# Performance work log

Hardware: AMD Instinct MI355X
Metric: run time of the kernel (lower is better)

The kernel has to match this reference:

```python
import jax, jax.numpy as jnp
import numpy as np

B, H, S, D = 2, 12, 2048, 64

def setup_inputs() -> dict:
    key = jax.random.key(0)
    kq, kk, kv = jax.random.split(key, 3)
    Q = jax.random.normal(kq, (B, H, S, D), dtype=jnp.float32)
    K = jax.random.normal(kk, (B, H, S, D), dtype=jnp.float32)
    V = jax.random.normal(kv, (B, H, S, D), dtype=jnp.float32)
    return {"Q": Q, "K": K, "V": V}

def reference(Q, K, V):
    # NOTE: original code scales by sqrt(Q.shape[-2]) (the sequence length),
    # not the head dim — reproduced faithfully.
    scale = 1.0 / np.sqrt(Q.shape[-2]).astype(np.float32)
    scores = jnp.einsum('bhqd,bhkd->bhqk', Q, K) * scale  # [B,H,S,S]
    attn = jax.nn.softmax(scores, axis=-1)
    context = jnp.einsum('bhqk,bhkd->bhqd', attn, V)      # [B,H,S,D]
    # torch .squeeze(-1) only removes the last dim if it is size 1; D=64 so no-op
    return context
```

## Files before the change

### kernel.cpp

```cpp
#include <hip/hip_runtime.h>
#include <hip/hip_bf16.h>
#include <math.h>
#include <stdint.h>

#define BATCH 2
#define NH 12
#define SEQ 2048
#define HD 64
#define TQ 64
#define TK 64
#define NHEADS (BATCH*NH)
#define NIT (SEQ / TK)

typedef short bf16x8 __attribute__((ext_vector_type(8)));
typedef float f32x4 __attribute__((ext_vector_type(4)));
typedef unsigned short us8_t __attribute__((ext_vector_type(8)));

#if __has_builtin(__builtin_amdgcn_exp2f)
#define EXP2F(x) __builtin_amdgcn_exp2f(x)
#else
#define EXP2F(x) exp2f(x)
#endif

static __device__ __forceinline__ unsigned short f2bf(float f) {
    unsigned int u = __float_as_uint(f);
    u += 0x7fffu + ((u >> 16) & 1u);
    return (unsigned short)(u >> 16);
}

static __device__ __forceinline__ unsigned int pack2bf(float a, float b) {
    __hip_bfloat162 v = __float22bfloat162_rn(float2{a, b});
    return *(unsigned int*)&v;
}

static __device__ __forceinline__ void async_cp16(const void* g, void* l) {
    __builtin_amdgcn_global_load_lds(
        (const __attribute__((address_space(1))) void*)g,
        (__attribute__((address_space(3))) void*)(uintptr_t)l,
        16, 0, 0);
}

__global__ __launch_bounds__(256)
void prep_qkv(const float* __restrict__ Q, const float* __restrict__ K,
              const float* __restrict__ V,
              unsigned short* __restrict__ Qb, unsigned short* __restrict__ Kb,
              unsigned short* __restrict__ Vtb, float qs) {
    const int bh = blockIdx.x >> 5;
    const int s0 = (blockIdx.x & 31) * 64;
    const int tid = threadIdx.x;
    const size_t off = ((size_t)bh * SEQ + s0) * HD;

    #pragma unroll
    for (int i = 0; i < 2; ++i) {
        size_t e0 = off + (size_t)(tid + 256 * i) * 8;
        float4 a = *(const float4*)&Q[e0];
        float4 b = *(const float4*)&Q[e0 + 4];
        us8_t rq = { f2bf(a.x*qs), f2bf(a.y*qs), f2bf(a.z*qs), f2bf(a.w*qs),
                     f2bf(b.x*qs), f2bf(b.y*qs), f2bf(b.z*qs), f2bf(b.w*qs) };
        *(us8_t*)&Qb[e0] = rq;
        float4 c = *(const float4*)&K[e0];
        float4 d = *(const float4*)&K[e0 + 4];
        us8_t rk = { f2bf(c.x), f2bf(c.y), f2bf(c.z), f2bf(c.w),
                     f2bf(d.x), f2bf(d.y), f2bf(d.z), f2bf(d.w) };
        *(us8_t*)&Kb[e0] = rk;
    }

    const float* Vsrc = V + off;
    unsigned short* Vdst = Vtb + (size_t)bh * HD * SEQ;
    const int n  = tid & 63;
    const int cg = tid >> 6;
    #pragma unroll
    for (int i = 0; i < 4; ++i) {
        int c4 = (cg + 4 * i) * 4;
        float4 v = *(const float4*)&Vsrc[(size_t)n * HD + c4];
        Vdst[(size_t)(c4 + 0) * SEQ + s0 + n] = f2bf(v.x);
        Vdst[(size_t)(c4 + 1) * SEQ + s0 + n] = f2bf(v.y);
        Vdst[(size_t)(c4 + 2) * SEQ + s0 + n] = f2bf(v.z);
        Vdst[(size_t)(c4 + 3) * SEQ + s0 + n] = f2bf(v.w);
    }
}

__global__ __launch_bounds__(128)
void fa_main(const unsigned short* __restrict__ Qb,
             const unsigned short* __restrict__ Kb,
             const unsigned short* __restrict__ Vtb,
             float* __restrict__ O) {
    const int x  = blockIdx.x & 7;
    const int t  = blockIdx.x >> 3;
    const int bh = x + 8 * (t % 3);
    const int qt = t / 3;
    const int q0 = qt * TQ;

    __shared__ unsigned short Ks[TK * HD];
    __shared__ unsigned short Vs[HD * TK];
    __shared__ unsigned short QP[2 * 32 * 72];
    __shared__ float Lw[2][32];

    const int tid  = threadIdx.x;
    const int w    = tid >> 6;
    const int lane = tid & 63;
    const int col  = lane & 15;
    const int quad = lane >> 4;
    const int r8   = lane >> 3;
    const int c8   = lane & 7;
    const int swz  = col & 7;

    const unsigned short* Qh = Qb  + ((size_t)bh * SEQ + q0) * HD;
    const unsigned short* Kh = Kb  + (size_t)bh * SEQ * HD;
    const unsigned short* Vh = Vtb + (size_t)bh * HD * SEQ;

    #pragma unroll
    for (int i = 0; i < 4; ++i) {
        const int R = w * 32 + i * 8;
        async_cp16(Qh + (size_t)(R + r8) * HD + (c8 ^ r8) * 8, &QP[R * HD]);
    }
    #pragma unroll
    for (int i = 0; i < 4; ++i) {
        const int R = w * 32 + i * 8;
        async_cp16(Kh + (size_t)(R + r8) * HD + (c8 ^ r8) * 8, &Ks[R * HD]);
        async_cp16(Vh + (size_t)(R + r8) * SEQ + (c8 ^ r8) * 8, &Vs[R * HD]);
    }
    __syncthreads();

    bf16x8 qf[2][2];
    #pragma unroll
    for (int mt = 0; mt < 2; ++mt)
        #pragma unroll
        for (int ks = 0; ks < 2; ++ks)
            qf[mt][ks] = *(const bf16x8*)&QP[(w*32 + mt*16 + col) * HD + (((ks*4 + quad) ^ swz) * 8)];
    __syncthreads();

    unsigned short* Psw = &QP[w * 2304];

    f32x4 o[2][4];
    #pragma unroll
    for (int mt = 0; mt < 2; ++mt)
        #pragma unroll
        for (int dt = 0; dt < 4; ++dt) o[mt][dt] = (f32x4){0.f, 0.f, 0.f, 0.f};
    float lsum[2] = {0.f, 0.f};

    for (int it = 0; it < NIT; ++it) {
        f32x4 sc[2][4];
        #pragma unroll
        for (int nt = 0; nt < 4; ++nt) {
            const int kr = (nt*16 + col) * HD;
            bf16x8 kf0 = *(const bf16x8*)&Ks[kr + (((0*4 + quad) ^ swz) * 8)];
            bf16x8 kf1 = *(const bf16x8*)&Ks[kr + (((1*4 + quad) ^ swz) * 8)];
            #pragma unroll
            for (int mt = 0; mt < 2; ++mt) {
                f32x4 z = {0.f, 0.f, 0.f, 0.f};
                z = __builtin_amdgcn_mfma_f32_16x16x32_bf16(kf0, qf[mt][0], z, 0, 0, 0);
                z = __builtin_amdgcn_mfma_f32_16x16x32_bf16(kf1, qf[mt][1], z, 0, 0, 0);
                sc[mt][nt] = z;
            }
        }

        #pragma unroll
        for (int mt = 0; mt < 2; ++mt) {
            #pragma unroll
            for (int nt = 0; nt < 4; ++nt) {
                float p0 = EXP2F(sc[mt][nt][0]);
                float p1 = EXP2F(sc[mt][nt][1]);
                float p2 = EXP2F(sc[mt][nt][2]);
                float p3 = EXP2F(sc[mt][nt][3]);
                lsum[mt] += (p0 + p1) + (p2 + p3);
                uint2 pk = { pack2bf(p0, p1), pack2bf(p2, p3) };
                *(uint2*)&Psw[(mt*16 + col) * 72 + nt*16 + quad*4] = pk;
            }
        }

        bf16x8 pf[2][2];
        #pragma unroll
        for (int mt = 0; mt < 2; ++mt)
            #pragma unroll
            for (int ks = 0; ks < 2; ++ks)
                pf[mt][ks] = *(const bf16x8*)&Psw[(mt*16 + col) * 72 + ks*32 + quad*8];
        #pragma unroll
        for (int dt = 0; dt < 4; ++dt) {
            const int vr = (dt*16 + col) * HD;
            bf16x8 vf0 = *(const bf16x8*)&Vs[vr + (((0*4 + quad) ^ swz) * 8)];
            bf16x8 vf1 = *(const bf16x8*)&Vs[vr + (((1*4 + quad) ^ swz) * 8)];
            #pragma unroll
            for (int mt = 0; mt < 2; ++mt) {
                o[mt][dt] = __builtin_amdgcn_mfma_f32_16x16x32_bf16(pf[mt][0], vf0, o[mt][dt], 0, 0, 0);
                o[mt][dt] = __builtin_amdgcn_mfma_f32_16x16x32_bf16(pf[mt][1], vf1, o[mt][dt], 0, 0, 0);
            }
        }

        __syncthreads();
        if (it + 1 < NIT) {
            const int kv0 = (it + 1) * TK;
            #pragma unroll
            for (int i = 0; i < 4; ++i) {
                const int R = w * 32 + i * 8;
                async_cp16(Kh + (size_t)(kv0 + R + r8) * HD  + (c8 ^ r8) * 8, &Ks[R * HD]);
                async_cp16(Vh + (size_t)(R + r8) * SEQ + kv0 + (c8 ^ r8) * 8, &Vs[R * HD]);
            }
        }
        __syncthreads();
    }

    #pragma unroll
    for (int mt = 0; mt < 2; ++mt) {
        lsum[mt] += __shfl_xor(lsum[mt], 16, 64);
        lsum[mt] += __shfl_xor(lsum[mt], 32, 64);
    }
    if (quad == 0) {
        Lw[w][col]      = lsum[0];
        Lw[w][16 + col] = lsum[1];
    }
    float* Oh = O + ((size_t)bh * SEQ + q0 + w*32) * HD;
    #pragma unroll
    for (int mt = 0; mt < 2; ++mt) {
        #pragma unroll
        for (int r = 0; r < 4; ++r) {
            const int row = mt*16 + quad*4 + r;
            float inv = 1.0f / Lw[w][row];
            #pragma unroll
            for (int dt = 0; dt < 4; ++dt)
                Oh[(size_t)row * HD + dt*16 + col] = o[mt][dt][r] * inv;
        }
    }
}

#define PAD 8
#define LSTR (HD + PAD)

__global__ __launch_bounds__(256)
void fa_fwd_fb(const float* __restrict__ Q, const float* __restrict__ K,
               const float* __restrict__ V, float* __restrict__ O) {
    const int x  = blockIdx.x & 7;
    const int t  = blockIdx.x >> 3;
    const int bh = x + 8 * (t % 3);
    const int qt = t / 3;
    const int q0 = qt * TQ;
    const long base = (long)bh * SEQ * HD;

    __shared__ unsigned short Qs[TQ][LSTR];
    __shared__ unsigned short Ks2[TK][LSTR];
    __shared__ unsigned short Vt[HD][TK + PAD];
    __shared__ unsigned short Ps2[4][16][LSTR];

    const int tid  = threadIdx.x;
    const int wave = tid >> 6;
    const int lane = tid & 63;
    const int col  = lane & 15;
    const int quad = lane >> 4;
    const int m0   = wave * 16;

    #pragma unroll
    for (int i = 0; i < 4; ++i) {
        int idx = tid + 256 * i;
        int row = idx >> 4;
        int c4  = (idx & 15) * 4;
        float4 v = *(const float4*)&Q[base + (long)(q0 + row) * HD + c4];
        ushort4 b = { f2bf(v.x), f2bf(v.y), f2bf(v.z), f2bf(v.w) };
        *(ushort4*)&Qs[row][c4] = b;
    }
    __syncthreads();

    bf16x8 aq0 = *(const bf16x8*)&Qs[m0 + col][quad * 8];
    bf16x8 aq1 = *(const bf16x8*)&Qs[m0 + col][32 + quad * 8];

    f32x4 o0 = {0.f,0.f,0.f,0.f}, o1 = o0, o2 = o0, o3 = o0;
    float l[4] = {0.f, 0.f, 0.f, 0.f};
    const float scale = 0.022097086912079608f;

    for (int kv0 = 0; kv0 < SEQ; kv0 += TK) {
        __syncthreads();
        #pragma unroll
        for (int i = 0; i < 4; ++i) {
            int idx = tid + 256 * i;
            int row = idx >> 4;
            int c4  = (idx & 15) * 4;
            float4 kv = *(const float4*)&K[base + (long)(kv0 + row) * HD + c4];
            ushort4 kb = { f2bf(kv.x), f2bf(kv.y), f2bf(kv.z), f2bf(kv.w) };
            *(ushort4*)&Ks2[row][c4] = kb;
            float4 vv = *(const float4*)&V[base + (long)(kv0 + row) * HD + c4];
            Vt[c4 + 0][row] = f2bf(vv.x);
            Vt[c4 + 1][row] = f2bf(vv.y);
            Vt[c4 + 2][row] = f2bf(vv.z);
            Vt[c4 + 3][row] = f2bf(vv.w);
        }
        __syncthreads();

        f32x4 sc[4];
        #pragma unroll
        for (int n = 0; n < 4; ++n) {
            bf16x8 b0 = *(const bf16x8*)&Ks2[n * 16 + col][quad * 8];
            bf16x8 b1 = *(const bf16x8*)&Ks2[n * 16 + col][32 + quad * 8];
            f32x4 acc = {0.f,0.f,0.f,0.f};
            acc = __builtin_amdgcn_mfma_f32_16x16x32_bf16(aq0, b0, acc, 0, 0, 0);
            acc = __builtin_amdgcn_mfma_f32_16x16x32_bf16(aq1, b1, acc, 0, 0, 0);
            sc[n] = acc;
        }

        float tsum[4] = {0.f, 0.f, 0.f, 0.f};
        #pragma unroll
        for (int n = 0; n < 4; ++n) {
            #pragma unroll
            for (int r = 0; r < 4; ++r) {
                float p = __expf(sc[n][r] * scale);
                tsum[r] += p;
                Ps2[wave][quad * 4 + r][n * 16 + col] = f2bf(p);
            }
        }
        #pragma unroll
        for (int off = 1; off < 16; off <<= 1) {
            #pragma unroll
            for (int r = 0; r < 4; ++r) tsum[r] += __shfl_xor(tsum[r], off, 64);
        }
        #pragma unroll
        for (int r = 0; r < 4; ++r) l[r] += tsum[r];

        bf16x8 ap0 = *(const bf16x8*)&Ps2[wave][col][quad * 8];
        bf16x8 ap1 = *(const bf16x8*)&Ps2[wave][col][32 + quad * 8];
        #pragma unroll
        for (int n = 0; n < 4; ++n) {
            bf16x8 b0 = *(const bf16x8*)&Vt[n * 16 + col][quad * 8];
            bf16x8 b1 = *(const bf16x8*)&Vt[n * 16 + col][32 + quad * 8];
            f32x4* op = (n == 0) ? &o0 : (n == 1) ? &o1 : (n == 2) ? &o2 : &o3;
            *op = __builtin_amdgcn_mfma_f32_16x16x32_bf16(ap0, b0, *op, 0, 0, 0);
            *op = __builtin_amdgcn_mfma_f32_16x16x32_bf16(ap1, b1, *op, 0, 0, 0);
        }
    }

    float inv[4];
    #pragma unroll
    for (int r = 0; r < 4; ++r) inv[r] = 1.0f / l[r];
    #pragma unroll
    for (int r = 0; r < 4; ++r) {
        long row = base + (long)(q0 + m0 + quad * 4 + r) * HD;
        O[row +  0 + col] = o0[r] * inv[r];
        O[row + 16 + col] = o1[r] * inv[r];
        O[row + 32 + col] = o2[r] * inv[r];
        O[row + 48 + col] = o3[r] * inv[r];
    }
}

extern "C" void kernel_launch(void* const* d_in, const int* in_sizes, int n_in,
                              void* d_out, int out_size, void* d_ws, size_t ws_size,
                              hipStream_t stream) {
    const float* Q = (const float*)d_in[0];
    const float* K = (const float*)d_in[1];
    const float* V = (const float*)d_in[2];
    float* O = (float*)d_out;

    const size_t tensorElems = (size_t)NHEADS * SEQ * HD;
    const size_t need = 3 * tensorElems * sizeof(unsigned short);

    if (ws_size >= need) {
        unsigned short* Qb  = (unsigned short*)d_ws;
        unsigned short* Kb  = Qb + tensorElems;
        unsigned short* Vtb = Kb + tensorElems;
        const float qs = (float)(1.4426950408889634 / sqrt(2048.0));
        prep_qkv<<<dim3(NHEADS * (SEQ / 64)), dim3(256), 0, stream>>>(Q, K, V, Qb, Kb, Vtb, qs);
        fa_main<<<dim3(NHEADS * (SEQ / TQ)), dim3(128), 0, stream>>>(Qb, Kb, Vtb, O);
    } else {
        fa_fwd_fb<<<dim3(NHEADS * (SEQ / TQ)), dim3(256), 0, stream>>>(Q, K, V, O);
    }
}
```

Baseline: 140.1 us.

## Split KV tile across four waves with 32x32 MFMA and double-buffered K/V

```diff
diff --git a/kernel.cpp b/kernel.cpp
--- a/kernel.cpp
+++ b/kernel.cpp
@@ -14,6 +14,7 @@
 
 typedef short bf16x8 __attribute__((ext_vector_type(8)));
 typedef float f32x4 __attribute__((ext_vector_type(4)));
+typedef float f32x16 __attribute__((ext_vector_type(16)));
 typedef unsigned short us8_t __attribute__((ext_vector_type(8)));
 
 #if __has_builtin(__builtin_amdgcn_exp2f)
@@ -80,7 +81,7 @@
     }
 }
 
-__global__ __launch_bounds__(128)
+__global__ __launch_bounds__(256)
 void fa_main(const unsigned short* __restrict__ Qb,
              const unsigned short* __restrict__ Kb,
              const unsigned short* __restrict__ Vtb,
@@ -91,134 +92,142 @@
     const int qt = t / 3;
     const int q0 = qt * TQ;
 
-    __shared__ unsigned short Ks[TK * HD];
-    __shared__ unsigned short Vs[HD * TK];
-    __shared__ unsigned short QP[2 * 32 * 72];
-    __shared__ float Lw[2][32];
+    __shared__ unsigned short Ksh[2][TK * HD];
+    __shared__ unsigned short Vsh[2][HD * TK];
+    __shared__ unsigned short Ps[TQ * TK];
+    __shared__ float Lsum[TQ];
+    __shared__ float Linv[TQ];
 
     const int tid  = threadIdx.x;
     const int w    = tid >> 6;
+    const int mt   = w >> 1;
+    const int nt   = w & 1;
     const int lane = tid & 63;
-    const int col  = lane & 15;
-    const int quad = lane >> 4;
+    const int l31  = lane & 31;
+    const int hi   = lane >> 5;
+    const int l7   = lane & 7;
     const int r8   = lane >> 3;
     const int c8   = lane & 7;
-    const int swz  = col & 7;
 
     const unsigned short* Qh = Qb  + ((size_t)bh * SEQ + q0) * HD;
     const unsigned short* Kh = Kb  + (size_t)bh * SEQ * HD;
     const unsigned short* Vh = Vtb + (size_t)bh * HD * SEQ;
 
-    #pragma unroll
-    for (int i = 0; i < 4; ++i) {
-        const int R = w * 32 + i * 8;
-        async_cp16(Qh + (size_t)(R + r8) * HD + (c8 ^ r8) * 8, &QP[R * HD]);
-    }
-    #pragma unroll
-    for (int i = 0; i < 4; ++i) {
-        const int R = w * 32 + i * 8;
-        async_cp16(Kh + (size_t)(R + r8) * HD + (c8 ^ r8) * 8, &Ks[R * HD]);
-        async_cp16(Vh + (size_t)(R + r8) * SEQ + (c8 ^ r8) * 8, &Vs[R * HD]);
+    {
+        const int R = w * 16;
+        async_cp16(Qh + (size_t)(R     + r8) * HD + (c8 ^ r8) * 8, &Ksh[1][ R      * HD]);
+        async_cp16(Qh + (size_t)(R + 8 + r8) * HD + (c8 ^ r8) * 8, &Ksh[1][(R + 8) * HD]);
+        async_cp16(Kh + (size_t)(R     + r8) * HD + (c8 ^ r8) * 8, &Ksh[0][ R      * HD]);
+        async_cp16(Kh + (size_t)(R + 8 + r8) * HD + (c8 ^ r8) * 8, &Ksh[0][(R + 8) * HD]);
+        async_cp16(Vh + (size_t)(R     + r8) * SEQ + (c8 ^ r8) * 8, &Vsh[0][ R      * HD]);
+        async_cp16(Vh + (size_t)(R + 8 + r8) * SEQ + (c8 ^ r8) * 8, &Vsh[0][(R + 8) * HD]);
     }
     __syncthreads();
 
-    bf16x8 qf[2][2];
-    #pragma unroll
-    for (int mt = 0; mt < 2; ++mt)
-        #pragma unroll
-        for (int ks = 0; ks < 2; ++ks)
-            qf[mt][ks] = *(const bf16x8*)&QP[(w*32 + mt*16 + col) * HD + (((ks*4 + quad) ^ swz) * 8)];
+    bf16x8 qf[4];
+    #pragma unroll
+    for (int s = 0; s < 4; ++s)
+        qf[s] = *(const bf16x8*)&Ksh[1][(mt*32 + l31) * HD + (((s*2 + hi) ^ l7) * 8)];
     __syncthreads();
 
-    unsigned short* Psw = &QP[w * 2304];
-
-    f32x4 o[2][4];
-    #pragma unroll
-    for (int mt = 0; mt < 2; ++mt)
-        #pragma unroll
-        for (int dt = 0; dt < 4; ++dt) o[mt][dt] = (f32x4){0.f, 0.f, 0.f, 0.f};
-    float lsum[2] = {0.f, 0.f};
+    f32x16 o[2];
+    o[0] = (f32x16)(0.f);
+    o[1] = (f32x16)(0.f);
+    float lsum = 0.f;
 
     for (int it = 0; it < NIT; ++it) {
-        f32x4 sc[2][4];
-        #pragma unroll
-        for (int nt = 0; nt < 4; ++nt) {
-            const int kr = (nt*16 + col) * HD;
-            bf16x8 kf0 = *(const bf16x8*)&Ks[kr + (((0*4 + quad) ^ swz) * 8)];
-            bf16x8 kf1 = *(const bf16x8*)&Ks[kr + (((1*4 + quad) ^ swz) * 8)];
-            #pragma unroll
-            for (int mt = 0; mt < 2; ++mt) {
-                f32x4 z = {0.f, 0.f, 0.f, 0.f};
-                z = __builtin_amdgcn_mfma_f32_16x16x32_bf16(kf0, qf[mt][0], z, 0, 0, 0);
-                z = __builtin_amdgcn_mfma_f32_16x16x32_bf16(kf1, qf[mt][1], z, 0, 0, 0);
-                sc[mt][nt] = z;
+        const int cur = it & 1;
+        if (it + 1 < NIT) {
+            const int nb  = cur ^ 1;
+            const int kv0 = (it + 1) * TK;
+            const int R   = w * 16;
+            async_cp16(Kh + (size_t)(kv0 + R     + r8) * HD  + (c8 ^ r8) * 8, &Ksh[nb][ R      * HD]);
+            async_cp16(Kh + (size_t)(kv0 + R + 8 + r8) * HD  + (c8 ^ r8) * 8, &Ksh[nb][(R + 8) * HD]);
+            async_cp16(Vh + (size_t)(R     + r8) * SEQ + kv0 + (c8 ^ r8) * 8, &Vsh[nb][ R      * HD]);
+            async_cp16(Vh + (size_t)(R + 8 + r8) * SEQ + kv0 + (c8 ^ r8) * 8, &Vsh[nb][(R + 8) * HD]);
+        }
+        const unsigned short* Ks = Ksh[cur];
+        const unsigned short* Vs = Vsh[cur];
+
+        f32x16 sc = (f32x16)(0.f);
+        #pragma unroll
+        for (int s = 0; s < 4; ++s) {
+            bf16x8 kf = *(const bf16x8*)&Ks[(nt*32 + l31) * HD + (((s*2 + hi) ^ l7) * 8)];
+            sc = __builtin_amdgcn_mfma_f32_32x32x16_bf16(kf, qf[s], sc, 0, 0, 0);
+        }
+
+        float e[16];
+        #pragma unroll
+        for (int r = 0; r < 16; ++r) e[r] = EXP2F(sc[r]);
+        #pragma unroll
+        for (int r = 0; r < 16; ++r) lsum += e[r];
+        #pragma unroll
+        for (int g = 0; g < 4; ++g) {
+            const int m = mt*32 + l31;
+            const int ch = nt*4 + g;
+            uint2 pk = { pack2bf(e[4*g+0], e[4*g+1]), pack2bf(e[4*g+2], e[4*g+3]) };
+            *(uint2*)&Ps[m * TK + ((ch ^ (m & 7)) * 8) + hi * 4] = pk;
+        }
+
+        bf16x8 pf[2];
+        #pragma unroll
+        for (int ks = 0; ks < 2; ++ks) {
+            const int m = mt*32 + l31;
+            const int ch = nt*4 + ks*2 + hi;
+            pf[ks] = *(const bf16x8*)&Ps[m * TK + ((ch ^ (m & 7)) * 8)];
+        }
+        #pragma unroll
+        for (int dt = 0; dt < 2; ++dt) {
+            const int d = dt*32 + l31;
+            #pragma unroll
+            for (int ks = 0; ks < 2; ++ks) {
+                const int ch = nt*4 + ks*2 + hi;
+                bf16x8 vf = *(const bf16x8*)&Vs[d * HD + ((ch ^ l7) * 8)];
+                o[dt] = __builtin_amdgcn_mfma_f32_32x32x16_bf16(pf[ks], vf, o[dt], 0, 0, 0);
             }
         }
 
-        #pragma unroll
-        for (int mt = 0; mt < 2; ++mt) {
-            #pragma unroll
-            for (int nt = 0; nt < 4; ++nt) {
-                float p0 = EXP2F(sc[mt][nt][0]);
-                float p1 = EXP2F(sc[mt][nt][1]);
-                float p2 = EXP2F(sc[mt][nt][2]);
-                float p3 = EXP2F(sc[mt][nt][3]);
-                lsum[mt] += (p0 + p1) + (p2 + p3);
-                uint2 pk = { pack2bf(p0, p1), pack2bf(p2, p3) };
-                *(uint2*)&Psw[(mt*16 + col) * 72 + nt*16 + quad*4] = pk;
+        __syncthreads();
+    }
+
+    lsum += __shfl_xor(lsum, 32, 64);
+    float* ORed = (float*)Ksh;
+
+    if (nt == 1) {
+        if (lane < 32) Lsum[mt*32 + lane] = lsum;
+        #pragma unroll
+        for (int dt = 0; dt < 2; ++dt) {
+            const int d = dt*32 + l31;
+            #pragma unroll
+            for (int g = 0; g < 4; ++g) {
+                const int m0 = mt*32 + 8*g + 4*hi;
+                const int ph = (m0 >> 2) ^ (d & 15);
+                float4 v = { o[dt][4*g+0], o[dt][4*g+1], o[dt][4*g+2], o[dt][4*g+3] };
+                *(float4*)&ORed[d * 64 + ph * 4] = v;
             }
         }
-
-        bf16x8 pf[2][2];
-        #pragma unroll
-        for (int mt = 0; mt < 2; ++mt)
-            #pragma unroll
-            for (int ks = 0; ks < 2; ++ks)
-                pf[mt][ks] = *(const bf16x8*)&Psw[(mt*16 + col) * 72 + ks*32 + quad*8];
-        #pragma unroll
-        for (int dt = 0; dt < 4; ++dt) {
-            const int vr = (dt*16 + col) * HD;
-            bf16x8 vf0 = *(const bf16x8*)&Vs[vr + (((0*4 + quad) ^ swz) * 8)];
-            bf16x8 vf1 = *(const bf16x8*)&Vs[vr + (((1*4 + quad) ^ swz) * 8)];
-            #pragma unroll
-            for (int mt = 0; mt < 2; ++mt) {
-                o[mt][dt] = __builtin_amdgcn_mfma_f32_16x16x32_bf16(pf[mt][0], vf0, o[mt][dt], 0, 0, 0);
-                o[mt][dt] = __builtin_amdgcn_mfma_f32_16x16x32_bf16(pf[mt][1], vf1, o[mt][dt], 0, 0, 0);
+    }
+    __syncthreads();
+
+    if (nt == 0) {
+        float ltot = lsum + Lsum[mt*32 + l31];
+        if (lane < 32) Linv[mt*32 + lane] = 1.0f / ltot;
+        float* Oh = O + ((size_t)bh * SEQ + q0) * HD;
+        #pragma unroll
+        for (int dt = 0; dt < 2; ++dt) {
+            const int d = dt*32 + l31;
+            #pragma unroll
+            for (int g = 0; g < 4; ++g) {
+                const int m0 = mt*32 + 8*g + 4*hi;
+                const int ph = (m0 >> 2) ^ (d & 15);
+                float4 part = *(const float4*)&ORed[d * 64 + ph * 4];
+                float4 inv4 = *(const float4*)&Linv[m0];
+                const float* pp = (const float*)&part;
+                const float* ii = (const float*)&inv4;
+                #pragma unroll
+                for (int j = 0; j < 4; ++j)
+                    Oh[(size_t)(m0 + j) * HD + d] = (o[dt][4*g+j] + pp[j]) * ii[j];
             }
-        }
-
-        __syncthreads();
-        if (it + 1 < NIT) {
-            const int kv0 = (it + 1) * TK;
-            #pragma unroll
-            for (int i = 0; i < 4; ++i) {
-                const int R = w * 32 + i * 8;
-                async_cp16(Kh + (size_t)(kv0 + R + r8) * HD  + (c8 ^ r8) * 8, &Ks[R * HD]);
-                async_cp16(Vh + (size_t)(R + r8) * SEQ + kv0 + (c8 ^ r8) * 8, &Vs[R * HD]);
-            }
-        }
-        __syncthreads();
-    }
-
-    #pragma unroll
-    for (int mt = 0; mt < 2; ++mt) {
-        lsum[mt] += __shfl_xor(lsum[mt], 16, 64);
-        lsum[mt] += __shfl_xor(lsum[mt], 32, 64);
-    }
-    if (quad == 0) {
-        Lw[w][col]      = lsum[0];
-        Lw[w][16 + col] = lsum[1];
-    }
-    float* Oh = O + ((size_t)bh * SEQ + q0 + w*32) * HD;
-    #pragma unroll
-    for (int mt = 0; mt < 2; ++mt) {
-        #pragma unroll
-        for (int r = 0; r < 4; ++r) {
-            const int row = mt*16 + quad*4 + r;
-            float inv = 1.0f / Lw[w][row];
-            #pragma unroll
-            for (int dt = 0; dt < 4; ++dt)
-                Oh[(size_t)row * HD + dt*16 + col] = o[mt][dt][r] * inv;
         }
     }
 }
@@ -355,7 +364,7 @@
         unsigned short* Vtb = Kb + tensorElems;
         const float qs = (float)(1.4426950408889634 / sqrt(2048.0));
         prep_qkv<<<dim3(NHEADS * (SEQ / 64)), dim3(256), 0, stream>>>(Q, K, V, Qb, Kb, Vtb, qs);
-        fa_main<<<dim3(NHEADS * (SEQ / TQ)), dim3(128), 0, stream>>>(Qb, Kb, Vtb, O);
+        fa_main<<<dim3(NHEADS * (SEQ / TQ)), dim3(256), 0, stream>>>(Qb, Kb, Vtb, O);
     } else {
         fa_fwd_fb<<<dim3(NHEADS * (SEQ / TQ)), dim3(256), 0, stream>>>(Q, K, V, O);
     }
```

Result: faster. 126.5 us (-9.7%).
